# Kernel optimization log

Measured on AMD Instinct MI355X. Metric: run time of the kernel, lower is better.

## Reference

```python
import jax, jax.numpy as jnp
import numpy as np

B, T, D_MODEL, N_HEADS = 4, 2048, 1024, 16
HEAD_DIM = D_MODEL // N_HEADS  # 64
ROPE_BASE = 10000.0


def setup_inputs() -> dict:
    key = jax.random.key(0)
    k1, k2, k3 = jax.random.split(key, 3)
    x = jax.random.normal(k1, (B, T, D_MODEL), dtype=jnp.float32)
    # nn.Linear(d, 3d, bias=False) and nn.Linear(d, d, bias=False), stored as (in, out)
    w_qkv = jax.random.normal(k2, (D_MODEL, 3 * D_MODEL), dtype=jnp.float32) / np.sqrt(D_MODEL)
    w_proj = jax.random.normal(k3, (D_MODEL, D_MODEL), dtype=jnp.float32) / np.sqrt(D_MODEL)
    # standard RoPE tables: (T, HEAD_DIM/2)
    inv_freq = 1.0 / (ROPE_BASE ** (np.arange(0, HEAD_DIM, 2, dtype=np.float32) / HEAD_DIM))
    ang = np.arange(T, dtype=np.float32)[:, None] * inv_freq[None, :]
    cos = jnp.asarray(np.cos(ang), dtype=jnp.float32)
    sin = jnp.asarray(np.sin(ang), dtype=jnp.float32)
    return {"x": x, "cos": cos, "sin": sin, "w_qkv": w_qkv, "w_proj": w_proj}


def _apply_rope(x, cos, sin):
    # x: (B, H, T, D); cos/sin: (T, D/2) broadcast over (B, H)
    x1 = x[..., 0::2]
    x2 = x[..., 1::2]
    r1 = x1 * cos - x2 * sin
    r2 = x2 * cos + x1 * sin
    # interleave back: out[..., 0::2]=r1, out[..., 1::2]=r2
    return jnp.stack([r1, r2], axis=-1).reshape(x.shape)


def reference(x, cos, sin, w_qkv, w_proj):
    b, t, _ = x.shape
    qkv = (x @ w_qkv).reshape(b, t, 3, N_HEADS, HEAD_DIM).transpose(2, 0, 3, 1, 4)
    q, k, v = qkv[0], qkv[1], qkv[2]  # each (B, H, T, D)
    q = _apply_rope(q, cos[:t], sin[:t])
    k = _apply_rope(k, cos[:t], sin[:t])
    scale = 1.0 / jnp.sqrt(jnp.asarray(HEAD_DIM, dtype=x.dtype))
    scores = jnp.einsum("bhqd,bhkd->bhqk", q, k) * scale
    causal = jnp.tril(jnp.ones((t, t), dtype=bool))
    scores = jnp.where(causal, scores, jnp.finfo(scores.dtype).min)
    attn = jax.nn.softmax(scores, axis=-1)
    out = jnp.einsum("bhqk,bhkd->bhqd", attn, v)
    out = out.transpose(0, 2, 1, 3).reshape(b, t, D_MODEL)
    return out @ w_proj
```

## Files before the change

kernel.cpp:

```cpp
#include <hip/hip_runtime.h>
#include <cstdint>
#include <cstddef>

typedef __attribute__((ext_vector_type(8))) short bf16x8;
typedef __attribute__((ext_vector_type(4))) float f32x4;
typedef __attribute__((ext_vector_type(16))) float f32x16;
typedef __attribute__((ext_vector_type(4))) unsigned int u32x4;

#define B_ 4
#define T_ 2048
#define DM 1024
#define NH 16
#define HD 64

static __device__ __forceinline__ unsigned short f2bf(float f) {
  union { float f; unsigned int u; } v; v.f = f;
  unsigned int r = v.u + 0x7FFFu + ((v.u >> 16) & 1u);
  return (unsigned short)(r >> 16);
}
static __device__ __forceinline__ float b2f(unsigned short u) {
  union { unsigned int u; float f; } v; v.u = ((unsigned int)u) << 16;
  return v.f;
}
static __device__ __forceinline__ float exp2_fast(float x) {
  float r;
  asm volatile("v_exp_f32 %0, %1" : "=v"(r) : "v"(x));
  return r;
}
static __device__ __forceinline__ unsigned int pack_bf2(float a, float b) {
  return (unsigned int)f2bf(a) | ((unsigned int)f2bf(b) << 16);
}

static __device__ __forceinline__ void gll16(const void* g, void* l) {
  __builtin_amdgcn_global_load_lds(
      (const __attribute__((address_space(1))) void*)g,
      (__attribute__((address_space(3))) void*)l, 16, 0, 0);
}

#define BARRIER() do { asm volatile("" ::: "memory"); __builtin_amdgcn_s_barrier(); asm volatile("" ::: "memory"); } while (0)
#define WAITV0() asm volatile("s_waitcnt vmcnt(0)" ::: "memory")

__global__ void cast_f32_to_bf16(const float* __restrict__ in,
                                 unsigned short* __restrict__ out, int n8) {
  for (int i = blockIdx.x * blockDim.x + threadIdx.x; i < n8;
       i += gridDim.x * blockDim.x) {
    const float4* p = (const float4*)(in + (size_t)i * 8);
    float4 a = p[0], b = p[1];
    bf16x8 o;
    o[0] = f2bf(a.x); o[1] = f2bf(a.y); o[2] = f2bf(a.z); o[3] = f2bf(a.w);
    o[4] = f2bf(b.x); o[5] = f2bf(b.y); o[6] = f2bf(b.z); o[7] = f2bf(b.w);
    *(bf16x8*)(out + (size_t)i * 8) = o;
  }
}

__global__ void transpose_cast(const float* __restrict__ in,
                               unsigned short* __restrict__ out, int R, int C) {
  __shared__ unsigned short tile[32][33];
  int c0 = blockIdx.x * 32, r0 = blockIdx.y * 32;
  int tx = threadIdx.x, ty = threadIdx.y;
#pragma unroll
  for (int j = 0; j < 32; j += 8) {
    float v = in[(size_t)(r0 + ty + j) * C + c0 + tx];
    tile[tx][ty + j] = f2bf(v);
  }
  __syncthreads();
#pragma unroll
  for (int j = 0; j < 32; j += 8) {
    out[(size_t)(c0 + ty + j) * R + r0 + tx] = tile[ty + j][tx];
  }
}

#define GEMM_MAIN(As, Bs, Agl, Bgl, acc)                                     \
  {                                                                          \
    const char* gA = (const char*)(Agl) +                                    \
                     (size_t)(m0 + (tid >> 3)) * 2048 +                      \
                     (((tid & 7) ^ ((tid >> 3) & 7)) << 4);                  \
    const char* gB = (const char*)(Bgl) +                                    \
                     (size_t)(n0 + (tid >> 3)) * 2048 +                      \
                     (((tid & 7) ^ ((tid >> 3) & 7)) << 4);                  \
    for (int k0 = 0; k0 < 2048; k0 += 128) {                                 \
      _Pragma("unroll") for (int i = 0; i < 4; i++) {                        \
        gll16(gA + (size_t)i * 65536 + k0, (char*)(As) + i * 4096 + w * 1024);\
        gll16(gB + (size_t)i * 65536 + k0, (char*)(Bs) + i * 4096 + w * 1024);\
      }                                                                      \
      WAITV0();                                                              \
      BARRIER();                                                             \
      _Pragma("unroll") for (int kk = 0; kk < 2; kk++) {                     \
        bf16x8 af[4], bfr[4];                                                \
        const int ko = (kk * 64 + lg * 16) ^ ((lr & 7) << 4);                \
        _Pragma("unroll") for (int mi = 0; mi < 4; mi++)                     \
            af[mi] = *(const bf16x8*)((const char*)(As) +                    \
                                      (wr * 64 + mi * 16 + lr) * 128 + ko);  \
        _Pragma("unroll") for (int ni = 0; ni < 4; ni++)                     \
            bfr[ni] = *(const bf16x8*)((const char*)(Bs) +                   \
                                       (wc * 64 + ni * 16 + lr) * 128 + ko); \
        _Pragma("unroll") for (int mi = 0; mi < 4; mi++)                     \
            _Pragma("unroll") for (int ni = 0; ni < 4; ni++)                 \
                acc[mi][ni] = __builtin_amdgcn_mfma_f32_16x16x32_bf16(       \
                    af[mi], bfr[ni], acc[mi][ni], 0, 0, 0);                  \
      }                                                                      \
      BARRIER();                                                             \
    }                                                                        \
  }

__global__ __launch_bounds__(256, 3) void gemm_qkv(
    const unsigned short* __restrict__ A, const unsigned short* __restrict__ Bt,
    unsigned short* __restrict__ Qo, unsigned short* __restrict__ Ko,
    unsigned short* __restrict__ VTo) {
  __shared__ __align__(16) unsigned short As[128 * 64];
  __shared__ __align__(16) unsigned short Bs[128 * 64];
  const int bid = blockIdx.x;
  const int xcd = bid & 7;
  const int cc = bid >> 3;
  const int m0 = (xcd * 8 + cc / 24) * 128;
  const int n0 = (cc % 24) * 128;
  const int tid = threadIdx.x;
  const int w = tid >> 6, l = tid & 63;
  const int wr = w >> 1, wc = w & 1;
  const int lr = l & 15, lg = l >> 4;
  f32x4 acc[4][4];
#pragma unroll
  for (int i = 0; i < 4; i++)
#pragma unroll
    for (int j = 0; j < 4; j++) acc[i][j] = (f32x4)0.f;

  GEMM_MAIN(As, Bs, A, Bt, acc)

#pragma unroll
  for (int mi = 0; mi < 4; mi++) {
#pragma unroll
    for (int ni = 0; ni < 4; ni++) {
      int col = n0 + wc * 64 + ni * 16 + lr;
      int which = col >> 10, hd = col & 1023;
      int h = hd >> 6, d = hd & 63;
#pragma unroll
      for (int r = 0; r < 4; r++) {
        int row = m0 + wr * 64 + mi * 16 + lg * 4 + r;
        int b = row >> 11, tt = row & 2047;
        unsigned short bv = f2bf(acc[mi][ni][r]);
        size_t bh = (size_t)(b * NH + h);
        if (which == 0)
          Qo[(bh * T_ + tt) * HD + d] = bv;
        else if (which == 1)
          Ko[(bh * T_ + tt) * HD + d] = bv;
        else
          VTo[(bh * HD + d) * T_ + tt] = bv;
      }
    }
  }
}

__global__ __launch_bounds__(256, 3) void gemm_proj(
    const unsigned short* __restrict__ A, const unsigned short* __restrict__ Bt,
    float* __restrict__ C) {
  __shared__ __align__(16) unsigned short As[128 * 64];
  __shared__ __align__(16) unsigned short Bs[128 * 64];
  const int bid = blockIdx.x;
  const int xcd = bid & 7;
  const int cc = bid >> 3;
  const int m0 = (xcd * 8 + cc / 8) * 128;
  const int n0 = (cc % 8) * 128;
  const int tid = threadIdx.x;
  const int w = tid >> 6, l = tid & 63;
  const int wr = w >> 1, wc = w & 1;
  const int lr = l & 15, lg = l >> 4;
  f32x4 acc[4][4];
#pragma unroll
  for (int i = 0; i < 4; i++)
#pragma unroll
    for (int j = 0; j < 4; j++) acc[i][j] = (f32x4)0.f;

  GEMM_MAIN(As, Bs, A, Bt, acc)

#pragma unroll
  for (int mi = 0; mi < 4; mi++) {
#pragma unroll
    for (int ni = 0; ni < 4; ni++) {
      int col = n0 + wc * 64 + ni * 16 + lr;
#pragma unroll
      for (int r = 0; r < 4; r++) {
        int row = m0 + wr * 64 + mi * 16 + lg * 4 + r;
        C[(size_t)row * 1024 + col] = acc[mi][ni][r];
      }
    }
  }
}

__global__ void rope_kernel(unsigned short* __restrict__ Q,
                            unsigned short* __restrict__ K,
                            const float* __restrict__ cosT,
                            const float* __restrict__ sinT) {
  const int nchunk = B_ * NH * T_ * (HD / 8);
  for (int idx = blockIdx.x * blockDim.x + threadIdx.x; idx < 2 * nchunk;
       idx += gridDim.x * blockDim.x) {
    int which = idx >= nchunk;
    int c = which ? idx - nchunk : idx;
    unsigned short* base = which ? K : Q;
    int ch = c & 7;
    int row = c >> 3;
    int tt = row & (T_ - 1);
    bf16x8 v = *(bf16x8*)(base + (size_t)row * HD + ch * 8);
    const float4 cc4 = *(const float4*)(cosT + tt * 32 + ch * 4);
    const float4 ss4 = *(const float4*)(sinT + tt * 32 + ch * 4);
    const float* ccp = (const float*)&cc4;
    const float* ssp = (const float*)&ss4;
    float scale = which ? 1.0f : 0.18033688f;
#pragma unroll
    for (int p = 0; p < 4; p++) {
      float cc = ccp[p], ss = ssp[p];
      float x1 = b2f((unsigned short)v[2 * p]);
      float x2 = b2f((unsigned short)v[2 * p + 1]);
      v[2 * p] = (short)f2bf((x1 * cc - x2 * ss) * scale);
      v[2 * p + 1] = (short)f2bf((x2 * cc + x1 * ss) * scale);
    }
    *(bf16x8*)(base + (size_t)row * HD + ch * 8) = v;
  }
}

__global__ __launch_bounds__(256, 4) void attn_kernel(
    const unsigned short* __restrict__ Q, const unsigned short* __restrict__ K,
    const unsigned short* __restrict__ VT, unsigned short* __restrict__ O) {
  __shared__ __align__(16) unsigned short Ks[3][4096];
  __shared__ __align__(16) unsigned short Vs[2][4096];

  const int blk = blockIdx.x;
  const int j2 = blk >> 3;
  const int bh = (blk & 7) * 8 + (j2 & 7);
  const int qt = 15 - (j2 >> 3);
  const int b = bh >> 4, h = bh & 15;
  const int tid = threadIdx.x;
  const int w = tid >> 6, l = tid & 63;
  const int q31 = l & 31, h5 = l >> 5;
  const int q0w = qt * 128 + w * 32;
  const int q_abs = q0w + q31;

  const unsigned short* Qb = Q + (size_t)bh * T_ * HD;
  const char* Kc = (const char*)(K + (size_t)bh * T_ * HD);
  const char* Vc = (const char*)(VT + (size_t)bh * HD * T_);

  const int c0 = (w * 2) * 64 + l;
  const int c1 = (w * 2 + 1) * 64 + l;
  const int r0 = c0 >> 3, r1 = c1 >> 3;
  const int sw0 = ((c0 & 7) * 16) ^ ((r0 & 7) << 4);
  const int sw1 = ((c1 & 7) * 16) ^ ((r1 & 7) << 4);
  const char* pK0 = Kc + r0 * 128 + sw0;
  const char* pK1 = Kc + r1 * 128 + sw1;
  const char* pV0 = Vc + (size_t)r0 * (T_ * 2) + sw0;
  const char* pV1 = Vc + (size_t)r1 * (T_ * 2) + sw1;

#define SK(buf, tile)                                                       \
  do {                                                                      \
    size_t kb = (size_t)(tile) * 8192;                                      \
    gll16(pK0 + kb, (char*)Ks[buf] + (w * 2) * 1024);                       \
    gll16(pK1 + kb, (char*)Ks[buf] + (w * 2 + 1) * 1024);                   \
  } while (0)
#define SV(buf, tile)                                                       \
  do {                                                                      \
    size_t vb = (size_t)(tile) * 128;                                       \
    gll16(pV0 + vb, (char*)Vs[buf] + (w * 2) * 1024);                       \
    gll16(pV1 + vb, (char*)Vs[buf] + (w * 2 + 1) * 1024);                   \
  } while (0)

  bf16x8 qf[4];
#pragma unroll
  for (int ks4 = 0; ks4 < 4; ks4++)
    qf[ks4] = *(const bf16x8*)(Qb + (size_t)q_abs * HD + ks4 * 16 + h5 * 8);

  f32x16 ot0 = (f32x16)0.f, ot1 = (f32x16)0.f;
  float m_reg = -1e30f, lrow = 0.f;

  const int nt = 2 * qt + 2;
  const int jmax = q0w >> 6;

  SK(0, 0);
  SV(0, 0);
  if (nt > 1) {
    SV(1, 1);
    SK(1, 1);
  }
  if (nt > 2) SK(2, 2);

  int kcur = 0;
  for (int j = 0; j < nt; j++) {
    const int vcur = j & 1;
    if (j <= nt - 3) {
      asm volatile("s_waitcnt vmcnt(6)" ::: "memory");
    } else if (j == nt - 2) {
      asm volatile("s_waitcnt vmcnt(4)" ::: "memory");
    } else {
      asm volatile("s_waitcnt vmcnt(0)" ::: "memory");
    }
    BARRIER();
    if (j <= jmax) {
      f32x16 st[2];
      st[0] = (f32x16)0.f;
      st[1] = (f32x16)0.f;
      __builtin_amdgcn_s_setprio(1);
#pragma unroll
      for (int sub = 0; sub < 2; sub++) {
        const int row = sub * 32 + q31;
        const int sw = (row & 7) << 4;
#pragma unroll
        for (int ks4 = 0; ks4 < 4; ks4++) {
          bf16x8 kf = *(const bf16x8*)((const char*)Ks[kcur] + row * 128 +
                                       ((ks4 * 32 + h5 * 16) ^ sw));
          st[sub] = __builtin_amdgcn_mfma_f32_32x32x16_bf16(kf, qf[ks4],
                                                            st[sub], 0, 0, 0);
        }
      }
      __builtin_amdgcn_s_setprio(0);
      if (j == jmax) {
        const int t0 = j * 64;
#pragma unroll
        for (int sub = 0; sub < 2; sub++)
#pragma unroll
          for (int r = 0; r < 16; r++) {
            int kv_abs = t0 + sub * 32 + (r & 3) + 8 * (r >> 2) + 4 * h5;
            if (kv_abs > q_abs) st[sub][r] = -1e30f;
          }
      }
      float pmax = -1e30f;
#pragma unroll
      for (int sub = 0; sub < 2; sub++)
#pragma unroll
        for (int r = 0; r < 16; r++) pmax = fmaxf(pmax, st[sub][r]);
      pmax = fmaxf(pmax, __shfl_xor(pmax, 32, 64));
      const int defer = __all(pmax - m_reg <= 8.0f);
      if (!defer) {
        float mnew = fmaxf(m_reg, pmax);
        float alpha = exp2_fast(m_reg - mnew);
        m_reg = mnew;
        lrow *= alpha;
#pragma unroll
        for (int r = 0; r < 16; r++) {
          ot0[r] *= alpha;
          ot1[r] *= alpha;
        }
      }
      float rsum = 0.f;
#pragma unroll
      for (int sub = 0; sub < 2; sub++)
#pragma unroll
        for (int r = 0; r < 16; r++) {
          float p = exp2_fast(st[sub][r] - m_reg);
          st[sub][r] = p;
          rsum += p;
        }
      rsum += __shfl_xor(rsum, 32, 64);
      lrow += rsum;
      unsigned int pk[2][8];
#pragma unroll
      for (int sub = 0; sub < 2; sub++)
#pragma unroll
        for (int g = 0; g < 4; g++) {
          pk[sub][2 * g] = pack_bf2(st[sub][4 * g + 0], st[sub][4 * g + 1]);
          pk[sub][2 * g + 1] = pack_bf2(st[sub][4 * g + 2], st[sub][4 * g + 3]);
        }
      bf16x8 pf[4];
#pragma unroll
      for (int sub = 0; sub < 2; sub++)
#pragma unroll
        for (int s = 0; s < 2; s++) {
          unsigned int a0 = pk[sub][4 * s + 0], a1 = pk[sub][4 * s + 1];
          unsigned int b0 = pk[sub][4 * s + 2], b1 = pk[sub][4 * s + 3];
          unsigned int send0 = h5 ? a0 : b0, send1 = h5 ? a1 : b1;
          unsigned int sh0 = (unsigned int)__shfl_xor((int)send0, 32, 64);
          unsigned int sh1 = (unsigned int)__shfl_xor((int)send1, 32, 64);
          unsigned int ow0 = h5 ? b0 : a0, ow1 = h5 ? b1 : a1;
          u32x4 fu;
          fu[0] = h5 ? sh0 : ow0;
          fu[1] = h5 ? sh1 : ow1;
          fu[2] = h5 ? ow0 : sh0;
          fu[3] = h5 ? ow1 : sh1;
          pf[sub * 2 + s] = *(bf16x8*)&fu;
        }
      __builtin_amdgcn_s_setprio(1);
#pragma unroll
      for (int ks = 0; ks < 4; ks++) {
        const int colb = ks * 32 + h5 * 16;
        {
          const int row = q31;
          bf16x8 vf = *(const bf16x8*)((const char*)Vs[vcur] + row * 128 +
                                       (colb ^ ((row & 7) << 4)));
          ot0 = __builtin_amdgcn_mfma_f32_32x32x16_bf16(vf, pf[ks], ot0, 0, 0, 0);
        }
        {
          const int row = 32 + q31;
          bf16x8 vf = *(const bf16x8*)((const char*)Vs[vcur] + row * 128 +
                                       (colb ^ ((row & 7) << 4)));
          ot1 = __builtin_amdgcn_mfma_f32_32x32x16_bf16(vf, pf[ks], ot1, 0, 0, 0);
        }
      }
      __builtin_amdgcn_s_setprio(0);
    }
    BARRIER();
    if (j + 2 < nt) SV((j + 2) & 1, j + 2);
    if (j + 3 < nt) SK(kcur, j + 3);
    kcur = (kcur == 2) ? 0 : kcur + 1;
  }

  const float rcpl = 1.0f / lrow;
  unsigned short* Orow = O + ((size_t)b * T_ + q_abs) * DM + h * HD;
#pragma unroll
  for (int rg = 0; rg < 4; rg++) {
    ushort4 sv;
    sv.x = f2bf(ot0[4 * rg + 0] * rcpl);
    sv.y = f2bf(ot0[4 * rg + 1] * rcpl);
    sv.z = f2bf(ot0[4 * rg + 2] * rcpl);
    sv.w = f2bf(ot0[4 * rg + 3] * rcpl);
    *(ushort4*)(Orow + 8 * rg + 4 * h5) = sv;
    ushort4 sw_;
    sw_.x = f2bf(ot1[4 * rg + 0] * rcpl);
    sw_.y = f2bf(ot1[4 * rg + 1] * rcpl);
    sw_.z = f2bf(ot1[4 * rg + 2] * rcpl);
    sw_.w = f2bf(ot1[4 * rg + 3] * rcpl);
    *(ushort4*)(Orow + 32 + 8 * rg + 4 * h5) = sw_;
  }
#undef SK
#undef SV
}

extern "C" void kernel_launch(void* const* d_in, const int* in_sizes, int n_in,
                              void* d_out, int out_size, void* d_ws,
                              size_t ws_size, hipStream_t stream) {
  const float* x = (const float*)d_in[0];
  const float* cosT = (const float*)d_in[1];
  const float* sinT = (const float*)d_in[2];
  const float* w_qkv = (const float*)d_in[3];
  const float* w_proj = (const float*)d_in[4];
  float* out = (float*)d_out;

  char* ws = (char*)d_ws;
  unsigned short* x16 = (unsigned short*)(ws);
  unsigned short* wqkvT = (unsigned short*)(ws + (16 << 20));
  unsigned short* wprojT = (unsigned short*)(ws + (22 << 20));
  unsigned short* Qb = (unsigned short*)(ws + (24 << 20));
  unsigned short* Kb = (unsigned short*)(ws + (40 << 20));
  unsigned short* VTb = (unsigned short*)(ws + (56 << 20));
  unsigned short* Ob = x16;

  cast_f32_to_bf16<<<2048, 256, 0, stream>>>(x, x16, (B_ * T_ * DM) / 8);
  transpose_cast<<<dim3(3072 / 32, 1024 / 32), dim3(32, 8), 0, stream>>>(
      w_qkv, wqkvT, 1024, 3072);
  transpose_cast<<<dim3(1024 / 32, 1024 / 32), dim3(32, 8), 0, stream>>>(
      w_proj, wprojT, 1024, 1024);
  gemm_qkv<<<1536, 256, 0, stream>>>(x16, wqkvT, Qb, Kb, VTb);
  rope_kernel<<<4096, 256, 0, stream>>>(Qb, Kb, cosT, sinT);
  attn_kernel<<<1024, 256, 0, stream>>>(Qb, Kb, VTb, Ob);
  gemm_proj<<<512, 256, 0, stream>>>(Ob, wprojT, out);
}
```

Baseline: 202.2 us.

## Pipeline GEMM loads with 4-stage LDS ring, 8 waves, and fuse RoPE into QKV epilogue

Both GEMMs now use 512-thread blocks with a four-buffer LDS ring, prefetching three K-steps ahead with partial vmcnt waits, so global loads overlap MFMA work. Each wave computes a 64x32 tile instead of 64x64. RoPE and the Q scale are applied in the QKV GEMM epilogue by swapping pair values across lanes, which removes the separate rope kernel and its extra read/write pass over Q and K. The cost is 128KB of LDS per block, which limits occupancy to one block per CU.

```diff
diff --git a/kernel.cpp b/kernel.cpp
--- a/kernel.cpp
+++ b/kernel.cpp
@@ -38,7 +38,6 @@
 }
 
 #define BARRIER() do { asm volatile("" ::: "memory"); __builtin_amdgcn_s_barrier(); asm volatile("" ::: "memory"); } while (0)
-#define WAITV0() asm volatile("s_waitcnt vmcnt(0)" ::: "memory")
 
 __global__ void cast_f32_to_bf16(const float* __restrict__ in,
                                  unsigned short* __restrict__ out, int n8) {
@@ -70,45 +69,61 @@
   }
 }
 
-#define GEMM_MAIN(As, Bs, Agl, Bgl, acc)                                     \
+#define GEMM_PIPE(AsBuf, BsBuf, Agl, Bgl)                                    \
   {                                                                          \
-    const char* gA = (const char*)(Agl) +                                    \
-                     (size_t)(m0 + (tid >> 3)) * 2048 +                      \
-                     (((tid & 7) ^ ((tid >> 3) & 7)) << 4);                  \
-    const char* gB = (const char*)(Bgl) +                                    \
-                     (size_t)(n0 + (tid >> 3)) * 2048 +                      \
-                     (((tid & 7) ^ ((tid >> 3) & 7)) << 4);                  \
-    for (int k0 = 0; k0 < 2048; k0 += 128) {                                 \
-      _Pragma("unroll") for (int i = 0; i < 4; i++) {                        \
-        gll16(gA + (size_t)i * 65536 + k0, (char*)(As) + i * 4096 + w * 1024);\
-        gll16(gB + (size_t)i * 65536 + k0, (char*)(Bs) + i * 4096 + w * 1024);\
+    const int c0_ = w * 64 + l;                                              \
+    const int arow_ = c0_ >> 3;                                              \
+    const int asw_ = (((c0_ & 7) ^ (arow_ & 7)) << 4);                       \
+    const char* pA0 = (const char*)(Agl) + (size_t)(m0 + arow_) * 2048 + asw_;\
+    const char* pB0 = (const char*)(Bgl) + (size_t)(n0 + arow_) * 2048 + asw_;\
+    STG_(0, 0);                                                              \
+    STG_(1, 1);                                                              \
+    STG_(2, 2);                                                              \
+    for (int t = 0; t < 16; t++) {                                           \
+      if (t < 14)                                                            \
+        asm volatile("s_waitcnt vmcnt(8)" ::: "memory");                     \
+      else if (t == 14)                                                      \
+        asm volatile("s_waitcnt vmcnt(4)" ::: "memory");                     \
+      else                                                                   \
+        asm volatile("s_waitcnt vmcnt(0)" ::: "memory");                     \
+      BARRIER();                                                             \
+      if (t + 3 < 16) {                                                      \
+        STG_((t + 3) & 3, t + 3);                                            \
+        __builtin_amdgcn_sched_barrier(0);                                   \
       }                                                                      \
-      WAITV0();                                                              \
-      BARRIER();                                                             \
+      const char* Ab_ = (const char*)(AsBuf) + (t & 3) * 16384;              \
+      const char* Bb_ = (const char*)(BsBuf) + (t & 3) * 16384;              \
       _Pragma("unroll") for (int kk = 0; kk < 2; kk++) {                     \
-        bf16x8 af[4], bfr[4];                                                \
         const int ko = (kk * 64 + lg * 16) ^ ((lr & 7) << 4);                \
+        bf16x8 af[4], bfr[2];                                                \
         _Pragma("unroll") for (int mi = 0; mi < 4; mi++)                     \
-            af[mi] = *(const bf16x8*)((const char*)(As) +                    \
-                                      (wr * 64 + mi * 16 + lr) * 128 + ko);  \
-        _Pragma("unroll") for (int ni = 0; ni < 4; ni++)                     \
-            bfr[ni] = *(const bf16x8*)((const char*)(Bs) +                   \
-                                       (wc * 64 + ni * 16 + lr) * 128 + ko); \
+            af[mi] = *(const bf16x8*)(Ab_ + (wr * 64 + mi * 16 + lr) * 128 + ko); \
+        _Pragma("unroll") for (int ni = 0; ni < 2; ni++)                     \
+            bfr[ni] = *(const bf16x8*)(Bb_ + (wc * 32 + ni * 16 + lr) * 128 + ko); \
         _Pragma("unroll") for (int mi = 0; mi < 4; mi++)                     \
-            _Pragma("unroll") for (int ni = 0; ni < 4; ni++)                 \
+            _Pragma("unroll") for (int ni = 0; ni < 2; ni++)                 \
                 acc[mi][ni] = __builtin_amdgcn_mfma_f32_16x16x32_bf16(       \
                     af[mi], bfr[ni], acc[mi][ni], 0, 0, 0);                  \
       }                                                                      \
-      BARRIER();                                                             \
     }                                                                        \
   }
 
-__global__ __launch_bounds__(256, 3) void gemm_qkv(
+#define STG_(buf, t)                                                         \
+  do {                                                                       \
+    const size_t ko_ = (size_t)(t) * 128;                                    \
+    gll16(pA0 + ko_, (char*)AsB + (buf) * 16384 + w * 1024);                 \
+    gll16(pA0 + 131072 + ko_, (char*)AsB + (buf) * 16384 + 8192 + w * 1024); \
+    gll16(pB0 + ko_, (char*)BsB + (buf) * 16384 + w * 1024);                 \
+    gll16(pB0 + 131072 + ko_, (char*)BsB + (buf) * 16384 + 8192 + w * 1024); \
+  } while (0)
+
+__global__ __launch_bounds__(512, 1) void gemm_qkv(
     const unsigned short* __restrict__ A, const unsigned short* __restrict__ Bt,
+    const float* __restrict__ cosT, const float* __restrict__ sinT,
     unsigned short* __restrict__ Qo, unsigned short* __restrict__ Ko,
     unsigned short* __restrict__ VTo) {
-  __shared__ __align__(16) unsigned short As[128 * 64];
-  __shared__ __align__(16) unsigned short Bs[128 * 64];
+  __shared__ __align__(16) unsigned short AsB[4][8192];
+  __shared__ __align__(16) unsigned short BsB[4][8192];
   const int bid = blockIdx.x;
   const int xcd = bid & 7;
   const int cc = bid >> 3;
@@ -116,28 +131,39 @@
   const int n0 = (cc % 24) * 128;
   const int tid = threadIdx.x;
   const int w = tid >> 6, l = tid & 63;
-  const int wr = w >> 1, wc = w & 1;
+  const int wr = w >> 2, wc = w & 3;
   const int lr = l & 15, lg = l >> 4;
-  f32x4 acc[4][4];
+  f32x4 acc[4][2];
 #pragma unroll
   for (int i = 0; i < 4; i++)
 #pragma unroll
-    for (int j = 0; j < 4; j++) acc[i][j] = (f32x4)0.f;
-
-  GEMM_MAIN(As, Bs, A, Bt, acc)
+    for (int j = 0; j < 2; j++) acc[i][j] = (f32x4)0.f;
+
+  GEMM_PIPE(AsB, BsB, A, Bt)
 
 #pragma unroll
   for (int mi = 0; mi < 4; mi++) {
 #pragma unroll
-    for (int ni = 0; ni < 4; ni++) {
-      int col = n0 + wc * 64 + ni * 16 + lr;
-      int which = col >> 10, hd = col & 1023;
-      int h = hd >> 6, d = hd & 63;
+    for (int ni = 0; ni < 2; ni++) {
+      const int col = n0 + wc * 32 + ni * 16 + lr;
+      const int which = col >> 10;
+      const int hd = col & 1023;
+      const int h = hd >> 6, d = hd & 63;
+      const int fi = d >> 1;
+      const float sgn = (lr & 1) ? 1.0f : -1.0f;
+      const float qsc = (which == 0) ? 0.18033688f : 1.0f;
 #pragma unroll
       for (int r = 0; r < 4; r++) {
-        int row = m0 + wr * 64 + mi * 16 + lg * 4 + r;
-        int b = row >> 11, tt = row & 2047;
-        unsigned short bv = f2bf(acc[mi][ni][r]);
+        const int row = m0 + wr * 64 + mi * 16 + lg * 4 + r;
+        const int b = row >> 11, tt = row & 2047;
+        float v = acc[mi][ni][r];
+        if (which < 2) {
+          float p = __shfl_xor(v, 1, 64);
+          float cs = cosT[tt * 32 + fi];
+          float sn = sinT[tt * 32 + fi];
+          v = (v * cs + sgn * p * sn) * qsc;
+        }
+        unsigned short bv = f2bf(v);
         size_t bh = (size_t)(b * NH + h);
         if (which == 0)
           Qo[(bh * T_ + tt) * HD + d] = bv;
@@ -150,11 +176,11 @@
   }
 }
 
-__global__ __launch_bounds__(256, 3) void gemm_proj(
+__global__ __launch_bounds__(512, 1) void gemm_proj(
     const unsigned short* __restrict__ A, const unsigned short* __restrict__ Bt,
     float* __restrict__ C) {
-  __shared__ __align__(16) unsigned short As[128 * 64];
-  __shared__ __align__(16) unsigned short Bs[128 * 64];
+  __shared__ __align__(16) unsigned short AsB[4][8192];
+  __shared__ __align__(16) unsigned short BsB[4][8192];
   const int bid = blockIdx.x;
   const int xcd = bid & 7;
   const int cc = bid >> 3;
@@ -162,58 +188,27 @@
   const int n0 = (cc % 8) * 128;
   const int tid = threadIdx.x;
   const int w = tid >> 6, l = tid & 63;
-  const int wr = w >> 1, wc = w & 1;
+  const int wr = w >> 2, wc = w & 3;
   const int lr = l & 15, lg = l >> 4;
-  f32x4 acc[4][4];
+  f32x4 acc[4][2];
 #pragma unroll
   for (int i = 0; i < 4; i++)
 #pragma unroll
-    for (int j = 0; j < 4; j++) acc[i][j] = (f32x4)0.f;
-
-  GEMM_MAIN(As, Bs, A, Bt, acc)
+    for (int j = 0; j < 2; j++) acc[i][j] = (f32x4)0.f;
+
+  GEMM_PIPE(AsB, BsB, A, Bt)
 
 #pragma unroll
   for (int mi = 0; mi < 4; mi++) {
 #pragma unroll
-    for (int ni = 0; ni < 4; ni++) {
-      int col = n0 + wc * 64 + ni * 16 + lr;
+    for (int ni = 0; ni < 2; ni++) {
+      const int col = n0 + wc * 32 + ni * 16 + lr;
 #pragma unroll
       for (int r = 0; r < 4; r++) {
-        int row = m0 + wr * 64 + mi * 16 + lg * 4 + r;
+        const int row = m0 + wr * 64 + mi * 16 + lg * 4 + r;
         C[(size_t)row * 1024 + col] = acc[mi][ni][r];
       }
     }
-  }
-}
-
-__global__ void rope_kernel(unsigned short* __restrict__ Q,
-                            unsigned short* __restrict__ K,
-                            const float* __restrict__ cosT,
-                            const float* __restrict__ sinT) {
-  const int nchunk = B_ * NH * T_ * (HD / 8);
-  for (int idx = blockIdx.x * blockDim.x + threadIdx.x; idx < 2 * nchunk;
-       idx += gridDim.x * blockDim.x) {
-    int which = idx >= nchunk;
-    int c = which ? idx - nchunk : idx;
-    unsigned short* base = which ? K : Q;
-    int ch = c & 7;
-    int row = c >> 3;
-    int tt = row & (T_ - 1);
-    bf16x8 v = *(bf16x8*)(base + (size_t)row * HD + ch * 8);
-    const float4 cc4 = *(const float4*)(cosT + tt * 32 + ch * 4);
-    const float4 ss4 = *(const float4*)(sinT + tt * 32 + ch * 4);
-    const float* ccp = (const float*)&cc4;
-    const float* ssp = (const float*)&ss4;
-    float scale = which ? 1.0f : 0.18033688f;
-#pragma unroll
-    for (int p = 0; p < 4; p++) {
-      float cc = ccp[p], ss = ssp[p];
-      float x1 = b2f((unsigned short)v[2 * p]);
-      float x2 = b2f((unsigned short)v[2 * p + 1]);
-      v[2 * p] = (short)f2bf((x1 * cc - x2 * ss) * scale);
-      v[2 * p + 1] = (short)f2bf((x2 * cc + x1 * ss) * scale);
-    }
-    *(bf16x8*)(base + (size_t)row * HD + ch * 8) = v;
   }
 }
 
@@ -444,8 +439,7 @@
       w_qkv, wqkvT, 1024, 3072);
   transpose_cast<<<dim3(1024 / 32, 1024 / 32), dim3(32, 8), 0, stream>>>(
       w_proj, wprojT, 1024, 1024);
-  gemm_qkv<<<1536, 256, 0, stream>>>(x16, wqkvT, Qb, Kb, VTb);
-  rope_kernel<<<4096, 256, 0, stream>>>(Qb, Kb, cosT, sinT);
+  gemm_qkv<<<1536, 512, 0, stream>>>(x16, wqkvT, cosT, sinT, Qb, Kb, VTb);
   attn_kernel<<<1024, 256, 0, stream>>>(Qb, Kb, VTb, Ob);
-  gemm_proj<<<512, 256, 0, stream>>>(Ob, wprojT, out);
-}
+  gemm_proj<<<512, 512, 0, stream>>>(Ob, wprojT, out);
+}
```

Result: slower. 254.1 us (+25.6%).
